# Optimization experiments

Measured on AMD Instinct MI355X. Metric: run time of the kernel, lower is better.

## Reference

```python
import jax, jax.numpy as jnp
import numpy as np

# ---- config constants (TwoCompartmentLIFConfig defaults) ----
DT = 1.0                      # ms per Euler step
G_L, E_L = 0.05, 0.0          # somatic leak
G_L_D = 0.03                  # dendritic leak
C_D = 0.5                     # dendritic capacitance
G_C = 0.05                    # soma-dendrite coupling
E_E, E_I = 3.0, -0.5
E_NMDA, E_GABA_B = 3.0, -0.8
E_CA = 4.0
E_ADAPT = -0.5
V_TH, V_RESET, TAU_REF = 1.0, 0.0, 5.0
MG_K, MG_VHALF = 5.0, 0.5     # NMDA Mg2+ block sigmoid
THETA_CA, G_CA_SPIKE = 2.0, 0.3
BAP_AMP = 0.3
ADAPT_INC = 0.0
# conductance decay factors exp(-dt/tau)
D_E  = float(np.exp(-DT / 5.0))
D_I  = float(np.exp(-DT / 10.0))
D_N  = float(np.exp(-DT / 100.0))
D_GB = float(np.exp(-DT / 400.0))
D_CA = float(np.exp(-DT / 20.0))
D_AD = float(np.exp(-DT / 100.0))

T, N = 50, 500000
IN_SCALE = 0.06


def setup_inputs() -> dict:
    key = jax.random.key(0)
    ks = jax.random.split(key, 7)
    names = ["g_exc_basal", "g_inh_basal", "g_nmda_basal", "g_gaba_b_in",
             "g_exc_apical", "g_inh_apical", "g_nmda_apical"]
    return {n: IN_SCALE * jax.random.uniform(k, (T, N), dtype=jnp.float32)
            for n, k in zip(names, ks)}


def _run(g_exc_basal, g_inh_basal, g_nmda_basal, g_gaba_b_in,
         g_exc_apical, g_inh_apical, g_nmda_apical):
    n = g_exc_basal.shape[1]
    z = jnp.zeros((n,), jnp.float32)
    # carry: v_soma, v_dend, gEb, gIb, gNb, gGB, gEa, gIa, gNa, gCa, gAd, ref
    carry0 = (z + E_L, z + E_L, z, z, z, z, z, z, z, z, z, z)

    def step(carry, inp):
        v_s, v_d, gEb, gIb, gNb, gGB, gEa, gIa, gNa, gCa, gAd, ref = carry
        in_Eb, in_Ib, in_Nb, in_GB, in_Ea, in_Ia, in_Na = inp
        # decay + inject synaptic conductances
        gEb = gEb * D_E + in_Eb
        gIb = gIb * D_I + in_Ib
        gNb = gNb * D_N + in_Nb
        gGB = gGB * D_GB + in_GB
        gEa = gEa * D_E + in_Ea
        gIa = gIa * D_I + in_Ia
        gNa = gNa * D_N + in_Na
        gCa = gCa * D_CA
        # NMDA Mg2+ block gated at the LOCAL compartment voltage
        mg_s = jax.nn.sigmoid(MG_K * (v_s - MG_VHALF))
        mg_d = jax.nn.sigmoid(MG_K * (v_d - MG_VHALF))
        # somatic current (C_m = 1)
        I_s = (G_L * (E_L - v_s) + gEb * (E_E - v_s) + gIb * (E_I - v_s)
               + gNb * mg_s * (E_NMDA - v_s) + gGB * (E_GABA_B - v_s)
               + gAd * (E_ADAPT - v_s) + G_C * (v_d - v_s))
        # dendritic current
        I_d = (G_L_D * (E_L - v_d) + gEa * (E_E - v_d) + gIa * (E_I - v_d)
               + gNa * mg_d * (E_NMDA - v_d) + gCa * (E_CA - v_d)
               + G_C * (v_s - v_d))
        refractory = ref > 0.0
        v_s = jnp.where(refractory, V_RESET, v_s + DT * I_s)
        v_d = v_d + (DT / C_D) * I_d
        # spike + reset + refractory
        spike = (v_s >= V_TH) & jnp.logical_not(refractory)
        spike_f = spike.astype(jnp.float32)
        v_s = jnp.where(spike, V_RESET, v_s)
        ref = jnp.where(spike, TAU_REF, jnp.maximum(ref - DT, 0.0))
        gAd = gAd * D_AD + spike_f * ADAPT_INC
        # back-propagating AP depolarises dendrite
        v_d = jnp.where(spike, v_d + BAP_AMP * (E_CA - v_d), v_d)
        # dendritic Ca spike
        gCa = gCa + (v_d >= THETA_CA).astype(jnp.float32) * G_CA_SPIKE
        carry = (v_s, v_d, gEb, gIb, gNb, gGB, gEa, gIa, gNa, gCa, gAd, ref)
        return carry, (spike_f, v_s)

    inputs = (g_exc_basal, g_inh_basal, g_nmda_basal, g_gaba_b_in,
              g_exc_apical, g_inh_apical, g_nmda_apical)
    _, (spikes, v_trace) = jax.lax.scan(step, carry0, inputs)
    return spikes, v_trace  # each [T, N]


def reference(g_exc_basal, g_inh_basal, g_nmda_basal, g_gaba_b_in,
              g_exc_apical, g_inh_apical, g_nmda_apical):
    return _run(g_exc_basal, g_inh_basal, g_nmda_basal, g_gaba_b_in,
                g_exc_apical, g_inh_apical, g_nmda_apical)
```

## Files before the change

kernel.cpp:

```cpp
#include <hip/hip_runtime.h>
#include <math.h>

namespace {
constexpr float D_E   = 0.8187307530779818f;
constexpr float D_I   = 0.9048374180359595f;
constexpr float D_N   = 0.9900498337491681f;
constexpr float D_GB  = 0.9975031223974601f;
constexpr float D_CA  = 0.9512294245007140f;

constexpr float DT      = 1.0f;
constexpr float G_L     = 0.05f;
constexpr float E_L     = 0.0f;
constexpr float G_L_D   = 0.03f;
constexpr float DT_C_D  = 2.0f;
constexpr float G_C     = 0.05f;
constexpr float E_E     = 3.0f;
constexpr float E_I     = -0.5f;
constexpr float E_NMDA  = 3.0f;
constexpr float E_GABA_B= -0.8f;
constexpr float E_CA    = 4.0f;
constexpr float V_TH    = 1.0f;
constexpr float V_RESET = 0.0f;
constexpr float TAU_REF = 5.0f;
constexpr float MG_K    = 5.0f;
constexpr float MG_VHALF= 0.5f;
constexpr float THETA_CA= 2.0f;
constexpr float G_CA_SPIKE = 0.3f;
constexpr float BAP_AMP = 0.3f;
}

__device__ __forceinline__ void lif_step(
    float in_Eb, float in_Ib, float in_Nb, float in_GB,
    float in_Ea, float in_Ia, float in_Na,
    float& v_s, float& v_d,
    float& gEb, float& gIb, float& gNb, float& gGB,
    float& gEa, float& gIa, float& gNa, float& gCa, float& ref,
    float& spike_out, float& v_out)
{
    gEb = gEb * D_E  + in_Eb;
    gIb = gIb * D_I  + in_Ib;
    gNb = gNb * D_N  + in_Nb;
    gGB = gGB * D_GB + in_GB;
    gEa = gEa * D_E  + in_Ea;
    gIa = gIa * D_I  + in_Ia;
    gNa = gNa * D_N  + in_Na;
    gCa = gCa * D_CA;

    const float mg_s = 1.0f / (1.0f + expf(-MG_K * (v_s - MG_VHALF)));
    const float mg_d = 1.0f / (1.0f + expf(-MG_K * (v_d - MG_VHALF)));

    const float I_s = G_L * (E_L - v_s) + gEb * (E_E - v_s) + gIb * (E_I - v_s)
                    + gNb * mg_s * (E_NMDA - v_s) + gGB * (E_GABA_B - v_s)
                    + G_C * (v_d - v_s);
    const float I_d = G_L_D * (E_L - v_d) + gEa * (E_E - v_d) + gIa * (E_I - v_d)
                    + gNa * mg_d * (E_NMDA - v_d) + gCa * (E_CA - v_d)
                    + G_C * (v_s - v_d);

    const bool refractory = ref > 0.0f;
    v_s = refractory ? V_RESET : (v_s + DT * I_s);
    v_d = v_d + DT_C_D * I_d;

    const bool spike = (v_s >= V_TH) && !refractory;
    const float spike_f = spike ? 1.0f : 0.0f;
    v_s = spike ? V_RESET : v_s;
    ref = spike ? TAU_REF : fmaxf(ref - DT, 0.0f);
    v_d = spike ? (v_d + BAP_AMP * (E_CA - v_d)) : v_d;
    gCa = gCa + ((v_d >= THETA_CA) ? G_CA_SPIKE : 0.0f);

    spike_out = spike_f;
    v_out = v_s;
}

__global__ __launch_bounds__(256)
void lif_vec4_kernel(const float* __restrict__ pEb, const float* __restrict__ pIb,
                     const float* __restrict__ pNb, const float* __restrict__ pGB,
                     const float* __restrict__ pEa, const float* __restrict__ pIa,
                     const float* __restrict__ pNa,
                     float* __restrict__ out, int N, int T)
{
    const long long tid  = (long long)blockIdx.x * blockDim.x + threadIdx.x;
    const long long base = tid * 4;
    if (base >= N) return;

    float v_s[4] = {E_L, E_L, E_L, E_L};
    float v_d[4] = {E_L, E_L, E_L, E_L};
    float gEb[4] = {}, gIb[4] = {}, gNb[4] = {}, gGB[4] = {};
    float gEa[4] = {}, gIa[4] = {}, gNa[4] = {}, gCa[4] = {}, ref[4] = {};

    const size_t vtrace_off = (size_t)T * (size_t)N;

    for (int t = 0; t < T; ++t) {
        const size_t off = (size_t)t * (size_t)N + (size_t)base;
        const float4 iEb = *(const float4*)(pEb + off);
        const float4 iIb = *(const float4*)(pIb + off);
        const float4 iNb = *(const float4*)(pNb + off);
        const float4 iGB = *(const float4*)(pGB + off);
        const float4 iEa = *(const float4*)(pEa + off);
        const float4 iIa = *(const float4*)(pIa + off);
        const float4 iNa = *(const float4*)(pNa + off);
        const float* fEb = reinterpret_cast<const float*>(&iEb);
        const float* fIb = reinterpret_cast<const float*>(&iIb);
        const float* fNb = reinterpret_cast<const float*>(&iNb);
        const float* fGB = reinterpret_cast<const float*>(&iGB);
        const float* fEa = reinterpret_cast<const float*>(&iEa);
        const float* fIa = reinterpret_cast<const float*>(&iIa);
        const float* fNa = reinterpret_cast<const float*>(&iNa);

        float4 osp, ov;
        float* sp = reinterpret_cast<float*>(&osp);
        float* vv = reinterpret_cast<float*>(&ov);

        #pragma unroll
        for (int j = 0; j < 4; ++j) {
            lif_step(fEb[j], fIb[j], fNb[j], fGB[j], fEa[j], fIa[j], fNa[j],
                     v_s[j], v_d[j],
                     gEb[j], gIb[j], gNb[j], gGB[j],
                     gEa[j], gIa[j], gNa[j], gCa[j], ref[j],
                     sp[j], vv[j]);
        }

        *reinterpret_cast<float4*>(out + off)              = osp;
        *reinterpret_cast<float4*>(out + vtrace_off + off) = ov;
    }
}

__global__ __launch_bounds__(256)
void lif_scalar_kernel(const float* __restrict__ pEb, const float* __restrict__ pIb,
                       const float* __restrict__ pNb, const float* __restrict__ pGB,
                       const float* __restrict__ pEa, const float* __restrict__ pIa,
                       const float* __restrict__ pNa,
                       float* __restrict__ out, int N, int T)
{
    const long long i = (long long)blockIdx.x * blockDim.x + threadIdx.x;
    if (i >= N) return;

    float v_s = E_L, v_d = E_L;
    float gEb = 0, gIb = 0, gNb = 0, gGB = 0;
    float gEa = 0, gIa = 0, gNa = 0, gCa = 0, ref = 0;

    const size_t vtrace_off = (size_t)T * (size_t)N;

    for (int t = 0; t < T; ++t) {
        const size_t off = (size_t)t * (size_t)N + (size_t)i;
        float sp, vv;
        lif_step(pEb[off], pIb[off], pNb[off], pGB[off], pEa[off], pIa[off], pNa[off],
                 v_s, v_d, gEb, gIb, gNb, gGB, gEa, gIa, gNa, gCa, ref, sp, vv);
        out[off]              = sp;
        out[vtrace_off + off] = vv;
    }
}

extern "C" void kernel_launch(void* const* d_in, const int* in_sizes, int n_in,
                              void* d_out, int out_size, void* d_ws, size_t ws_size,
                              hipStream_t stream) {
    const float* pEb = (const float*)d_in[0];
    const float* pIb = (const float*)d_in[1];
    const float* pNb = (const float*)d_in[2];
    const float* pGB = (const float*)d_in[3];
    const float* pEa = (const float*)d_in[4];
    const float* pIa = (const float*)d_in[5];
    const float* pNa = (const float*)d_in[6];
    float* out = (float*)d_out;

    const int T = 50;
    const int N = in_sizes[0] / T;

    if ((N & 3) == 0) {
        const int threads = N / 4;
        const int blocks = (threads + 255) / 256;
        lif_vec4_kernel<<<blocks, 256, 0, stream>>>(pEb, pIb, pNb, pGB, pEa, pIa, pNa,
                                                    out, N, T);
    } else {
        const int blocks = (N + 255) / 256;
        lif_scalar_kernel<<<blocks, 256, 0, stream>>>(pEb, pIb, pNb, pGB, pEa, pIa, pNa,
                                                      out, N, T);
    }
}
```

Baseline: 172.3 us.

## Replace vec4 kernel with scalar-per-thread kernel using software prefetch of next step

```diff
diff --git a/kernel.cpp b/kernel.cpp
--- a/kernel.cpp
+++ b/kernel.cpp
@@ -71,67 +71,14 @@
     v_out = v_s;
 }
 
-__global__ __launch_bounds__(256)
-void lif_vec4_kernel(const float* __restrict__ pEb, const float* __restrict__ pIb,
-                     const float* __restrict__ pNb, const float* __restrict__ pGB,
-                     const float* __restrict__ pEa, const float* __restrict__ pIa,
-                     const float* __restrict__ pNa,
-                     float* __restrict__ out, int N, int T)
+__global__ __launch_bounds__(256, 8)
+void lif_scalar_pf_kernel(const float* __restrict__ pEb, const float* __restrict__ pIb,
+                          const float* __restrict__ pNb, const float* __restrict__ pGB,
+                          const float* __restrict__ pEa, const float* __restrict__ pIa,
+                          const float* __restrict__ pNa,
+                          float* __restrict__ out, int N, int T)
 {
-    const long long tid  = (long long)blockIdx.x * blockDim.x + threadIdx.x;
-    const long long base = tid * 4;
-    if (base >= N) return;
-
-    float v_s[4] = {E_L, E_L, E_L, E_L};
-    float v_d[4] = {E_L, E_L, E_L, E_L};
-    float gEb[4] = {}, gIb[4] = {}, gNb[4] = {}, gGB[4] = {};
-    float gEa[4] = {}, gIa[4] = {}, gNa[4] = {}, gCa[4] = {}, ref[4] = {};
-
-    const size_t vtrace_off = (size_t)T * (size_t)N;
-
-    for (int t = 0; t < T; ++t) {
-        const size_t off = (size_t)t * (size_t)N + (size_t)base;
-        const float4 iEb = *(const float4*)(pEb + off);
-        const float4 iIb = *(const float4*)(pIb + off);
-        const float4 iNb = *(const float4*)(pNb + off);
-        const float4 iGB = *(const float4*)(pGB + off);
-        const float4 iEa = *(const float4*)(pEa + off);
-        const float4 iIa = *(const float4*)(pIa + off);
-        const float4 iNa = *(const float4*)(pNa + off);
-        const float* fEb = reinterpret_cast<const float*>(&iEb);
-        const float* fIb = reinterpret_cast<const float*>(&iIb);
-        const float* fNb = reinterpret_cast<const float*>(&iNb);
-        const float* fGB = reinterpret_cast<const float*>(&iGB);
-        const float* fEa = reinterpret_cast<const float*>(&iEa);
-        const float* fIa = reinterpret_cast<const float*>(&iIa);
-        const float* fNa = reinterpret_cast<const float*>(&iNa);
-
-        float4 osp, ov;
-        float* sp = reinterpret_cast<float*>(&osp);
-        float* vv = reinterpret_cast<float*>(&ov);
-
-        #pragma unroll
-        for (int j = 0; j < 4; ++j) {
-            lif_step(fEb[j], fIb[j], fNb[j], fGB[j], fEa[j], fIa[j], fNa[j],
-                     v_s[j], v_d[j],
-                     gEb[j], gIb[j], gNb[j], gGB[j],
-                     gEa[j], gIa[j], gNa[j], gCa[j], ref[j],
-                     sp[j], vv[j]);
-        }
-
-        *reinterpret_cast<float4*>(out + off)              = osp;
-        *reinterpret_cast<float4*>(out + vtrace_off + off) = ov;
-    }
-}
-
-__global__ __launch_bounds__(256)
-void lif_scalar_kernel(const float* __restrict__ pEb, const float* __restrict__ pIb,
-                       const float* __restrict__ pNb, const float* __restrict__ pGB,
-                       const float* __restrict__ pEa, const float* __restrict__ pIa,
-                       const float* __restrict__ pNa,
-                       float* __restrict__ out, int N, int T)
-{
-    const long long i = (long long)blockIdx.x * blockDim.x + threadIdx.x;
+    const int i = blockIdx.x * blockDim.x + threadIdx.x;
     if (i >= N) return;
 
     float v_s = E_L, v_d = E_L;
@@ -140,13 +87,26 @@
 
     const size_t vtrace_off = (size_t)T * (size_t)N;
 
+    size_t off = (size_t)i;
+    float nEb = pEb[off], nIb = pIb[off], nNb = pNb[off], nGB = pGB[off];
+    float nEa = pEa[off], nIa = pIa[off], nNa = pNa[off];
+
     for (int t = 0; t < T; ++t) {
-        const size_t off = (size_t)t * (size_t)N + (size_t)i;
+        const float cEb = nEb, cIb = nIb, cNb = nNb, cGB = nGB;
+        const float cEa = nEa, cIa = nIa, cNa = nNa;
+
+        const size_t noff = off + ((t + 1 < T) ? (size_t)N : 0);
+        nEb = pEb[noff]; nIb = pIb[noff]; nNb = pNb[noff]; nGB = pGB[noff];
+        nEa = pEa[noff]; nIa = pIa[noff]; nNa = pNa[noff];
+
         float sp, vv;
-        lif_step(pEb[off], pIb[off], pNb[off], pGB[off], pEa[off], pIa[off], pNa[off],
-                 v_s, v_d, gEb, gIb, gNb, gGB, gEa, gIa, gNa, gCa, ref, sp, vv);
+        lif_step(cEb, cIb, cNb, cGB, cEa, cIa, cNa,
+                 v_s, v_d, gEb, gIb, gNb, gGB, gEa, gIa, gNa, gCa, ref,
+                 sp, vv);
+
         out[off]              = sp;
         out[vtrace_off + off] = vv;
+        off += (size_t)N;
     }
 }
 
@@ -165,14 +125,7 @@
     const int T = 50;
     const int N = in_sizes[0] / T;
 
-    if ((N & 3) == 0) {
-        const int threads = N / 4;
-        const int blocks = (threads + 255) / 256;
-        lif_vec4_kernel<<<blocks, 256, 0, stream>>>(pEb, pIb, pNb, pGB, pEa, pIa, pNa,
-                                                    out, N, T);
-    } else {
-        const int blocks = (N + 255) / 256;
-        lif_scalar_kernel<<<blocks, 256, 0, stream>>>(pEb, pIb, pNb, pGB, pEa, pIa, pNa,
-                                                      out, N, T);
-    }
+    const int blocks = (N + 255) / 256;
+    lif_scalar_pf_kernel<<<blocks, 256, 0, stream>>>(pEb, pIb, pNb, pGB, pEa, pIa, pNa,
+                                                     out, N, T);
 }
```

Result: slower. 180.8 us (+4.9%).
